# Kernel optimization log

Measured on AMD Instinct MI355X. Metric: run time of the kernel, lower is better.

Reference implementation:

```python
import jax, jax.numpy as jnp
import numpy as np

B, T, E = 512, 12, 1024   # batch, channels/seq, embed_dim
NH, HS = 8, 128           # num_heads, head_size (head_size=128 hard-coded in source)
H = NH * HS               # sLSTM hidden = 1024 (== E)


def _layer_norm(x, g, b, eps=1e-5):
    mu = x.mean(-1, keepdims=True)
    var = x.var(-1, keepdims=True)
    return (x - mu) * jax.lax.rsqrt(var + eps) * g + b


def _conv1d_same(x, w, b):
    # x: (B, C, L), w: (O, I, K) odd K, 'same' padding, stride 1
    k = w.shape[-1]
    p = (k - 1) // 2
    y = jax.lax.conv_general_dilated(x, w, (1,), [(p, p)],
                                     dimension_numbers=('NCH', 'OIH', 'NCH'))
    return y + b[None, :, None]


def setup_inputs():
    key = jax.random.key(0)
    ks = jax.random.split(key, 16)
    s = 0.02
    def nrm(k, shape, scale=s):
        return jax.random.normal(k, shape, jnp.float32) * scale
    return {
        'x': jax.random.normal(ks[0], (B, T, E), jnp.float32),
        'ln_g': jnp.ones((E,), jnp.float32), 'ln_b': jnp.zeros((E,), jnp.float32),
        'fc1_w': nrm(ks[1], (12, 12, 3)), 'fc1_b': jnp.zeros((12,), jnp.float32),
        'fc2_w': nrm(ks[2], (12, 12)), 'fc2_b': jnp.zeros((12,), jnp.float32),
        'conv1_w': nrm(ks[3], (48, 12, 3)), 'conv1_b': jnp.zeros((48,), jnp.float32),
        'conv2_w': nrm(ks[4], (12, 48, 3)), 'conv2_b': jnp.zeros((12,), jnp.float32),
        'xl_ln_g': jnp.ones((E,), jnp.float32), 'xl_ln_b': jnp.zeros((E,), jnp.float32),
        'Wg': nrm(ks[5], (E, 4 * H)), 'bg': jnp.zeros((4 * H,), jnp.float32),
        'Rg': nrm(ks[6], (NH, 4 * HS, HS)),
        'gn_g': jnp.ones((H,), jnp.float32), 'gn_b': jnp.zeros((H,), jnp.float32),
        'upl_w': nrm(ks[7], (H, H)), 'upl_b': jnp.zeros((H,), jnp.float32),
        'upr_w': nrm(ks[8], (H, H)), 'upr_b': jnp.zeros((H,), jnp.float32),
        'down_w': nrm(ks[9], (H, E)), 'down_b': jnp.zeros((E,), jnp.float32),
    }


def _slstm_block(x, xl_ln_g, xl_ln_b, Wg, bg, Rg, gn_g, gn_b,
                 upl_w, upl_b, upr_w, upr_b, down_w, down_b):
    # Stabilized multi-head sLSTM block: pre-LN -> sLSTM recurrence (exp i/f gates
    # with max-stabilizer m), per-head GroupNorm, gated up/down proj (proj_factor=1),
    # residual. Recurrent weights are block-diagonal per head (NH, 4*HS, HS).
    xn = _layer_norm(x, xl_ln_g, xl_ln_b)
    gx = jnp.einsum('bte,eg->btg', xn, Wg) + bg            # (B,T,4H) input gate pre-acts
    gx = jnp.swapaxes(gx, 0, 1)                            # (T,B,4H)

    def step(carry, g_t):
        h, c, n, m = carry                                 # each (B,NH,HS)
        rec = jnp.einsum('bnh,ngh->bng', h, Rg)            # (B,NH,4HS)
        g = g_t.reshape(g_t.shape[0], NH, 4 * HS) + rec
        z_, i_, f_, o_ = jnp.split(g, 4, axis=-1)
        z = jnp.tanh(z_)
        o = jax.nn.sigmoid(o_)
        m_new = jnp.maximum(f_ + m, i_)                    # log-space stabilizer
        i = jnp.exp(i_ - m_new)
        f = jnp.exp(f_ + m - m_new)
        c = f * c + i * z
        n = f * n + i
        h = o * (c / n)
        return (h, c, n, m_new), h

    zero = jnp.zeros((x.shape[0], NH, HS), x.dtype)
    _, hseq = jax.lax.scan(step, (zero, zero, zero, zero), gx)
    h = jnp.swapaxes(hseq, 0, 1)                           # (B,T,NH,HS)
    # GroupNorm(num_groups=NH) over each head's HS channels
    mu = h.mean(-1, keepdims=True)
    var = h.var(-1, keepdims=True)
    hn = (h - mu) * jax.lax.rsqrt(var + 1e-5)
    hn = hn.reshape(x.shape[0], x.shape[1], H) * gn_g + gn_b
    left = jax.nn.gelu(hn @ upl_w + upl_b, approximate=False)
    right = hn @ upr_w + upr_b
    return (left * right) @ down_w + down_b + x


def reference(x, ln_g, ln_b, fc1_w, fc1_b, fc2_w, fc2_b, conv1_w, conv1_b,
              conv2_w, conv2_b, xl_ln_g, xl_ln_b, Wg, bg, Rg, gn_g, gn_b,
              upl_w, upl_b, upr_w, upr_b, down_w, down_b):
    xn = _layer_norm(x, ln_g, ln_b)
    skip = xn
    xc = _conv1d_same(xn, fc1_w, fc1_b)                    # fc1: Conv1d(12,12,3,'same')
    x1 = jnp.einsum('bcl,oc->bol', xc, fc2_w) + fc2_b[None, :, None]  # fc2: 1x1 conv
    x1 = _slstm_block(x1, xl_ln_g, xl_ln_b, Wg, bg, Rg, gn_g, gn_b,
                      upl_w, upl_b, upr_w, upr_b, down_w, down_b)
    # dropout(0.2) is identity in eval mode
    y = jax.nn.silu(xc) * x1 + skip
    z = _conv1d_same(y, conv1_w, conv1_b)                  # 12 -> 48
    z = _layer_norm(jax.nn.gelu(z, approximate=False), ln_g, ln_b)
    z = _conv1d_same(z, conv2_w, conv2_b)                  # 48 -> 12
    return z + skip
```

## Files before the change

### kernel.cpp

```cpp
#include <hip/hip_runtime.h>
#include <math.h>


typedef short short8_t __attribute__((ext_vector_type(8)));
typedef float floatx4 __attribute__((ext_vector_type(4)));
typedef float float2_t __attribute__((ext_vector_type(2)));

typedef unsigned int u32;
typedef const __attribute__((address_space(1))) u32 gu32;
typedef __attribute__((address_space(3))) u32 lu32;

static __device__ __forceinline__ float b2f(unsigned short u) {
    unsigned v = ((unsigned)u) << 16;
    return __builtin_bit_cast(float, v);
}
static __device__ __forceinline__ unsigned short f2b(float f) {
    unsigned u = __builtin_bit_cast(unsigned, f);
    u += 0x7FFFu + ((u >> 16) & 1u);
    return (unsigned short)(u >> 16);
}
static __device__ __forceinline__ float2_t make2u(unsigned u) {
    float2_t r;
    r.x = __builtin_bit_cast(float, u << 16);
    r.y = __builtin_bit_cast(float, u & 0xFFFF0000u);
    return r;
}
static __device__ __forceinline__ u32 pack2(float a, float b) {
    return ((u32)f2b(b) << 16) | (u32)f2b(a);
}
static __device__ __forceinline__ float gelu_fast(float x) {
    float u = 0.7978845608f * x * (1.f + 0.044715f * x * x);
    u = fminf(fmaxf(u, -9.f), 9.f);
    return x * __builtin_amdgcn_rcpf(1.f + __expf(-2.f * u));
}


__global__ __launch_bounds__(256) void transpose_bf16_k(
    const float* __restrict__ src, unsigned short* __restrict__ dst,
    int K, int N, int GS, int GO)
{
    __shared__ unsigned short tl[32][33];
    const int n0 = blockIdx.x * 32, k0 = blockIdx.y * 32;
    const int tx = threadIdx.x & 31, ty = threadIdx.x >> 5;
#pragma unroll
    for (int r = 0; r < 4; r++) {
        int k = ty + r * 8;
        tl[tx][k] = f2b(src[(size_t)(k0 + k) * N + n0 + tx]);
    }
    __syncthreads();
#pragma unroll
    for (int r = 0; r < 4; r++) {
        int n = n0 + ty * 4 + r;
        size_t row = (size_t)((n >> 4) * GS + GO + (n & 15));
        dst[row * K + k0 + tx] = tl[ty * 4 + r][tx];
    }
}

__global__ __launch_bounds__(256) void bias_ilv_kernel(
    const float* __restrict__ bl, const float* __restrict__ br,
    float* __restrict__ o)
{
    int i = blockIdx.x * 256 + threadIdx.x;
    int grp = i >> 5, w = i & 31;
    o[i] = (w < 16) ? bl[grp * 16 + w] : br[grp * 16 + (w - 16)];
}


template <int BF16OUT>
__global__ __launch_bounds__(256) void ln_kernel(
    const float* __restrict__ in, const float* __restrict__ g,
    const float* __restrict__ be, void* __restrict__ outp)
{
    const int row = blockIdx.x;
    const float* xr = in + (size_t)row * 1024;
    const int t = threadIdx.x;
    float v[4];
    float s = 0.f, ss = 0.f;
#pragma unroll
    for (int u = 0; u < 4; u++) {
        float q = xr[t + u * 256];
        v[u] = q; s += q; ss += q * q;
    }
#pragma unroll
    for (int off = 32; off >= 1; off >>= 1) {
        s += __shfl_xor(s, off);
        ss += __shfl_xor(ss, off);
    }
    __shared__ float red[8];
    const int wv = t >> 6, la = t & 63;
    if (la == 0) { red[wv] = s; red[4 + wv] = ss; }
    __syncthreads();
    s = red[0] + red[1] + red[2] + red[3];
    ss = red[4] + red[5] + red[6] + red[7];
    float mu = s * (1.f / 1024.f);
    float var = ss * (1.f / 1024.f) - mu * mu;
    float rs = rsqrtf(var + 1e-5f);
#pragma unroll
    for (int u = 0; u < 4; u++) {
        int i = t + u * 256;
        float yv = (v[u] - mu) * rs * g[i] + be[i];
        if (BF16OUT)
            ((unsigned short*)outp)[(size_t)row * 1024 + i] = f2b(yv);
        else
            ((float*)outp)[(size_t)row * 1024 + i] = yv;
    }
}


__global__ __launch_bounds__(512, 3) void ln_fc_kernel(
    const float* __restrict__ x,
    const float* __restrict__ g, const float* __restrict__ be,
    const float* __restrict__ w1, const float* __restrict__ b1,
    const float* __restrict__ w2, const float* __restrict__ b2,
    float* __restrict__ xn, float* __restrict__ xc, float* __restrict__ x1)
{
    __shared__ float sX[12][1028];
    __shared__ float sMR[12][2];
    const int b = blockIdx.x;
    const int t = threadIdx.x;
    const int p = t;
    const size_t boff = (size_t)b * 12288;

    if (t < 12) { sX[t][0] = 0.f; sX[t][1025] = 0.f; sX[t][1026] = 0.f; sX[t][1027] = 0.f; }
    {
        const float* gx = x + boff;
#pragma unroll
        for (int ci = 0; ci < 12; ci++) {
            sX[ci][1 + p] = gx[ci * 1024 + p];
            sX[ci][1 + p + 512] = gx[ci * 1024 + p + 512];
        }
    }
    __syncthreads();

    {
        const int wv = t >> 6, la = t & 63;
#pragma unroll
        for (int j = 0; j < 2; j++) {
            const int ch = wv + j * 8;
            if (ch < 12) {
                float s = 0.f, ss = 0.f;
#pragma unroll
                for (int u = 0; u < 16; u++) {
                    float v = sX[ch][1 + la + u * 64];
                    s += v; ss += v * v;
                }
#pragma unroll
                for (int off = 32; off >= 1; off >>= 1) {
                    s += __shfl_xor(s, off);
                    ss += __shfl_xor(ss, off);
                }
                if (la == 0) {
                    float mu = s * (1.f / 1024.f);
                    float var = ss * (1.f / 1024.f) - mu * mu;
                    sMR[ch][0] = mu;
                    sMR[ch][1] = rsqrtf(var + 1e-5f);
                }
            }
        }
    }
    __syncthreads();

    const float gA = g[p], bA = be[p];
    const float gB = g[p + 512], bB = be[p + 512];
#pragma unroll
    for (int ch = 0; ch < 12; ch++) {
        const float mu = sMR[ch][0], rs = sMR[ch][1];
        float v0 = (sX[ch][1 + p] - mu) * rs * gA + bA;
        float v1 = (sX[ch][1 + p + 512] - mu) * rs * gB + bB;
        sX[ch][1 + p] = v0;
        sX[ch][1 + p + 512] = v1;
        xn[boff + (size_t)ch * 1024 + p] = v0;
        xn[boff + (size_t)ch * 1024 + p + 512] = v1;
    }
    __syncthreads();

    float2_t a1[12];
#pragma unroll
    for (int o = 0; o < 12; o++) { float bv = b1[o]; a1[o] = float2_t{bv, bv}; }
    for (int ci = 0; ci < 12; ci++) {
        float2_t vm = float2_t{sX[ci][p],     sX[ci][p + 512]};
        float2_t v0 = float2_t{sX[ci][p + 1], sX[ci][p + 513]};
        float2_t vp = float2_t{sX[ci][p + 2], sX[ci][p + 514]};
        const float* wp = w1 + ci * 3;
#pragma unroll
        for (int o = 0; o < 12; o++) {
            const float* wo = wp + o * 36;
            a1[o] += vm * wo[0] + v0 * wo[1] + vp * wo[2];
        }
    }
#pragma unroll
    for (int o = 0; o < 12; o++) {
        xc[boff + (size_t)o * 1024 + p] = a1[o].x;
        xc[boff + (size_t)o * 1024 + p + 512] = a1[o].y;
    }

    float2_t a2[12];
#pragma unroll
    for (int o = 0; o < 12; o++) { float bv = b2[o]; a2[o] = float2_t{bv, bv}; }
#pragma unroll
    for (int ci = 0; ci < 12; ci++) {
#pragma unroll
        for (int o = 0; o < 12; o++)
            a2[o] += a1[ci] * w2[o * 12 + ci];
    }
#pragma unroll
    for (int o = 0; o < 12; o++) {
        x1[boff + (size_t)o * 1024 + p] = a2[o].x;
        x1[boff + (size_t)o * 1024 + p + 512] = a2[o].y;
    }
}


template <int MODE>
__global__ __launch_bounds__(256) void gemm_kernel(
    const unsigned short* __restrict__ A, const unsigned short* __restrict__ BT,
    const float* __restrict__ bias, void* __restrict__ out,
    int M, int N, int K,
    const float* __restrict__ xc, const float* __restrict__ x1,
    const float* __restrict__ skip)
{
    __shared__ __align__(16) unsigned short sA[128 * 32];
    __shared__ __align__(16) unsigned short sB[128 * 32];
    const int t = threadIdx.x;
    const int m0 = blockIdx.y * 128;
    const int n0 = blockIdx.x * 128;
    const int w = t >> 6;
    const int lane = t & 63;
    const int wr = (w >> 1) * 64;
    const int wc = (w & 1) * 64;
    const int lrow = lane & 15;
    const int quad = lane >> 4;
    const int row_l = t >> 2;
    const int cs = (t & 3) * 8;

    const unsigned short* gA0 = A + (size_t)(m0 + row_l) * K + cs;
    const unsigned short* gA1 = A + (size_t)(m0 + row_l + 64) * K + cs;
    const unsigned short* gB0 = BT + (size_t)(n0 + row_l) * K + cs;
    const unsigned short* gB1 = BT + (size_t)(n0 + row_l + 64) * K + cs;
    unsigned short* lA0 = sA + w * 512;
    unsigned short* lA1 = sA + 2048 + w * 512;
    unsigned short* lB0 = sB + w * 512;
    unsigned short* lB1 = sB + 2048 + w * 512;

    floatx4 acc[4][4];
#pragma unroll
    for (int i = 0; i < 4; i++)
#pragma unroll
        for (int j = 0; j < 4; j++) acc[i][j] = (floatx4)0.f;

    for (int k0 = 0; k0 < K; k0 += 32) {
        __syncthreads();
        __builtin_amdgcn_global_load_lds((gu32*)(gA0 + k0), (lu32*)lA0, 16, 0, 0);
        __builtin_amdgcn_global_load_lds((gu32*)(gA1 + k0), (lu32*)lA1, 16, 0, 0);
        __builtin_amdgcn_global_load_lds((gu32*)(gB0 + k0), (lu32*)lB0, 16, 0, 0);
        __builtin_amdgcn_global_load_lds((gu32*)(gB1 + k0), (lu32*)lB1, 16, 0, 0);
        __syncthreads();
        short8_t af[4], bfr[4];
#pragma unroll
        for (int i = 0; i < 4; i++) {
            af[i] = *(const short8_t*)(sA + (wr + i * 16 + lrow) * 32 + quad * 8);
            bfr[i] = *(const short8_t*)(sB + (wc + i * 16 + lrow) * 32 + quad * 8);
        }
#pragma unroll
        for (int i = 0; i < 4; i++)
#pragma unroll
            for (int j = 0; j < 4; j++)
                acc[i][j] = __builtin_amdgcn_mfma_f32_16x16x32_bf16(
                    af[i], bfr[j], acc[i][j], 0, 0, 0);
    }

    if (MODE == 3) {
#pragma unroll
        for (int i = 0; i < 4; i++) {
#pragma unroll
            for (int k = 0; k < 2; k++) {
#pragma unroll
                for (int r = 0; r < 4; r++) {
                    const int gm = m0 + wr + i * 16 + quad * 4 + r;
                    const int pl = n0 + wc + k * 32 + lrow;
                    float lv = acc[i][2 * k][r] + bias[pl];
                    float rv = acc[i][2 * k + 1][r] + bias[pl + 16];
                    const int nlog = (pl >> 5) * 16 + lrow;
                    ((unsigned short*)out)[(size_t)gm * (N >> 1) + nlog] =
                        f2b(gelu_fast(lv) * rv);
                }
            }
        }
    } else {
#pragma unroll
        for (int i = 0; i < 4; i++) {
#pragma unroll
            for (int j = 0; j < 4; j++) {
#pragma unroll
                for (int r = 0; r < 4; r++) {
                    const int gm = m0 + wr + i * 16 + quad * 4 + r;
                    const int gn = n0 + wc + j * 16 + lrow;
                    const size_t idx = (size_t)gm * N + gn;
                    float v = acc[i][j][r] + bias[gn];
                    if (MODE == 0) {
                        ((unsigned short*)out)[idx] = f2b(v);
                    } else {
                        float xcv = xc[idx];
                        float sig = xcv * __builtin_amdgcn_rcpf(1.f + __expf(-xcv));
                        ((unsigned short*)out)[idx] =
                            f2b(sig * (v + x1[idx]) + skip[idx]);
                    }
                }
            }
        }
    }
}


#define RECP 516
#define HBP  136

__global__ __launch_bounds__(1024, 1) void slstm_rec_kernel(
    const float* __restrict__ Rg,
    const unsigned short* __restrict__ gxb,
    const float* __restrict__ gn_g, const float* __restrict__ gn_b,
    unsigned short* __restrict__ hnb)
{
    __shared__ __align__(16) float sRec[16 * RECP];
    __shared__ __align__(16) unsigned short sHb[16 * HBP];
    const int head = blockIdx.x;
    const int b0 = blockIdx.y * 16;
    const int t = threadIdx.x;
    const int w = t >> 6;
    const int lane = t & 63;
    const int quad = lane >> 4;
    const int l16 = lane & 15;

    short8_t Bf[2][4];
    {
        const float* Rh = Rg + (size_t)head * 65536;
#pragma unroll
        for (int jt = 0; jt < 2; jt++)
#pragma unroll
            for (int kk = 0; kk < 4; kk++) {
                const float* src =
                    Rh + (size_t)(w * 32 + jt * 16 + l16) * 128 + kk * 32 + quad * 8;
                short8_t v;
#pragma unroll
                for (int j = 0; j < 8; j++) v[j] = (short)f2b(src[j]);
                Bf[jt][kk] = v;
            }
    }

    for (int i = t; i < 16 * HBP; i += 1024) sHb[i] = 0;

    const int la = lane;
    float c0 = 0.f, n0s = 0.f, m0 = 0.f;
    float c1 = 0.f, n1s = 0.f, m1 = 0.f;
    const float gg0 = gn_g[head * 128 + la];
    const float gg1 = gn_g[head * 128 + la + 64];
    const float gb0 = gn_b[head * 128 + la];
    const float gb1 = gn_b[head * 128 + la + 64];

    __syncthreads();

    for (int step = 0; step < 12; step++) {
        const unsigned short* gp =
            gxb + ((size_t)(b0 + w) * 12 + step) * 4096 + head * 512;
        float gz0 = b2f(gp[la]),       gz1 = b2f(gp[64 + la]);
        float gi0 = b2f(gp[128 + la]), gi1 = b2f(gp[192 + la]);
        float gf0 = b2f(gp[256 + la]), gf1 = b2f(gp[320 + la]);
        float go0 = b2f(gp[384 + la]), go1 = b2f(gp[448 + la]);

        short8_t Af[4];
#pragma unroll
        for (int kk = 0; kk < 4; kk++)
            Af[kk] = *(const short8_t*)(sHb + l16 * HBP + kk * 32 + quad * 8);
        floatx4 D0 = (floatx4)0.f, D1 = (floatx4)0.f;
#pragma unroll
        for (int kk = 0; kk < 4; kk++) {
            D0 = __builtin_amdgcn_mfma_f32_16x16x32_bf16(Af[kk], Bf[0][kk], D0, 0, 0, 0);
            D1 = __builtin_amdgcn_mfma_f32_16x16x32_bf16(Af[kk], Bf[1][kk], D1, 0, 0, 0);
        }
#pragma unroll
        for (int r = 0; r < 4; r++) {
            sRec[(quad * 4 + r) * RECP + w * 32 + l16] = D0[r];
            sRec[(quad * 4 + r) * RECP + w * 32 + 16 + l16] = D1[r];
        }
        __syncthreads();

        const float* rr = sRec + w * RECP;
        float zp0 = gz0 + rr[la],       zp1 = gz1 + rr[64 + la];
        float ip0 = gi0 + rr[128 + la], ip1 = gi1 + rr[192 + la];
        float fp0 = gf0 + rr[256 + la], fp1 = gf1 + rr[320 + la];
        float op0 = go0 + rr[384 + la], op1 = go1 + rr[448 + la];

        float e20 = __expf(-2.f * zp0), e21 = __expf(-2.f * zp1);
        float z0 = 2.f * __builtin_amdgcn_rcpf(1.f + e20) - 1.f;
        float z1 = 2.f * __builtin_amdgcn_rcpf(1.f + e21) - 1.f;
        float o0 = __builtin_amdgcn_rcpf(1.f + __expf(-op0));
        float o1 = __builtin_amdgcn_rcpf(1.f + __expf(-op1));
        float mn0 = fmaxf(fp0 + m0, ip0), mn1 = fmaxf(fp1 + m1, ip1);
        float ie0 = __expf(ip0 - mn0), ie1 = __expf(ip1 - mn1);
        float fe0 = __expf(fp0 + m0 - mn0), fe1 = __expf(fp1 + m1 - mn1);
        c0 = fe0 * c0 + ie0 * z0;  c1 = fe1 * c1 + ie1 * z1;
        n0s = fe0 * n0s + ie0;     n1s = fe1 * n1s + ie1;
        m0 = mn0;                  m1 = mn1;
        float h0 = o0 * c0 * __builtin_amdgcn_rcpf(n0s);
        float h1 = o1 * c1 * __builtin_amdgcn_rcpf(n1s);

        float s = h0 + h1, ss = h0 * h0 + h1 * h1;
#pragma unroll
        for (int off = 32; off >= 1; off >>= 1) {
            s += __shfl_xor(s, off);
            ss += __shfl_xor(ss, off);
        }
        float mu = s * (1.f / 128.f);
        float var = ss * (1.f / 128.f) - mu * mu;
        float rs = rsqrtf(var + 1e-5f);
        size_t base = ((size_t)(b0 + w) * 12 + step) * 1024 + head * 128;
        hnb[base + la] = f2b((h0 - mu) * rs * gg0 + gb0);
        hnb[base + la + 64] = f2b((h1 - mu) * rs * gg1 + gb1);

        sHb[w * HBP + la] = f2b(h0);
        sHb[w * HBP + la + 64] = f2b(h1);
        __syncthreads();
    }
}


__global__ __launch_bounds__(512, 6) void tail_fused_kernel(
    const unsigned short* __restrict__ y, const float* __restrict__ skip,
    const float* __restrict__ w1, const float* __restrict__ b1,
    const float* __restrict__ w2, const float* __restrict__ b2,
    const float* __restrict__ lng, const float* __restrict__ lnb,
    float* __restrict__ out)
{
    __shared__ unsigned short sY[12][1026];
    __shared__ unsigned short sZ[12][1026];
    __shared__ float sMR[12][2];
    const int b = blockIdx.x;
    const int t = threadIdx.x;
    const int p = t;
    const size_t boff = (size_t)b * 12288;

    {
        const u32* gy = (const u32*)(y + boff);
#pragma unroll
        for (int ci = 0; ci < 12; ci++)
            ((u32*)&sY[ci][0])[t] = gy[ci * 512 + t];
    }
    const float lgA = lng[2 * t], lbA = lnb[2 * t];
    const float lgB = lng[2 * t + 1], lbB = lnb[2 * t + 1];
    __syncthreads();

    float2_t acc[12];
#pragma unroll
    for (int o = 0; o < 12; o++) { float bv = b2[o]; acc[o] = float2_t{bv, bv}; }

    for (int q = 0; q < 4; q++) {
        float2_t a1[12];
#pragma unroll
        for (int o = 0; o < 12; o++) {
            float bo = b1[q * 12 + o];
            a1[o] = float2_t{bo, bo};
        }
        for (int ci = 0; ci < 12; ci++) {
            float2_t v0 = float2_t{b2f(sY[ci][p]), b2f(sY[ci][p + 512])};
            float2_t vm = float2_t{(p > 0) ? b2f(sY[ci][p - 1]) : 0.f,
                                   b2f(sY[ci][p + 511])};
            float2_t vp = float2_t{b2f(sY[ci][p + 1]),
                                   (p < 511) ? b2f(sY[ci][p + 513]) : 0.f};
            const float* wp = w1 + ci * 3;
#pragma unroll
            for (int o = 0; o < 12; o++) {
                const float* wo = wp + (q * 12 + o) * 36;
                a1[o] += vm * wo[0] + v0 * wo[1] + vp * wo[2];
            }
        }
#pragma unroll
        for (int o = 0; o < 12; o++) {
            sZ[o][p] = f2b(gelu_fast(a1[o].x));
            sZ[o][p + 512] = f2b(gelu_fast(a1[o].y));
        }
        __syncthreads();

        {
            const int wv = t >> 6, la = t & 63;
#pragma unroll
            for (int j = 0; j < 2; j++) {
                const int ch = wv + j * 8;
                if (ch < 12) {
                    float s = 0.f, ss = 0.f;
#pragma unroll
                    for (int u = 0; u < 8; u++) {
                        float2_t v = make2u(((const u32*)&sZ[ch][0])[la + u * 64]);
                        s += v.x + v.y;
                        ss += v.x * v.x + v.y * v.y;
                    }
#pragma unroll
                    for (int off = 32; off >= 1; off >>= 1) {
                        s += __shfl_xor(s, off);
                        ss += __shfl_xor(ss, off);
                    }
                    if (la == 0) {
                        float mu = s * (1.f / 1024.f);
                        float var = ss * (1.f / 1024.f) - mu * mu;
                        sMR[ch][0] = mu;
                        sMR[ch][1] = rsqrtf(var + 1e-5f);
                    }
                }
            }
        }
        __syncthreads();

#pragma unroll
        for (int ch = 0; ch < 12; ch++) {
            const float mu = sMR[ch][0], rs = sMR[ch][1];
            float2_t f = make2u(((const u32*)&sZ[ch][0])[t]);
            f.x = (f.x - mu) * rs * lgA + lbA;
            f.y = (f.y - mu) * rs * lgB + lbB;
            ((u32*)&sZ[ch][0])[t] = pack2(f.x, f.y);
        }
        __syncthreads();

        for (int ci = 0; ci < 12; ci++) {
            float2_t z0 = float2_t{b2f(sZ[ci][p]), b2f(sZ[ci][p + 512])};
            float2_t zm = float2_t{(p > 0) ? b2f(sZ[ci][p - 1]) : 0.f,
                                   b2f(sZ[ci][p + 511])};
            float2_t zp = float2_t{b2f(sZ[ci][p + 1]),
                                   (p < 511) ? b2f(sZ[ci][p + 513]) : 0.f};
            const float* wp = w2 + (q * 12 + ci) * 3;
#pragma unroll
            for (int o = 0; o < 12; o++)
                acc[o] += zm * wp[o * 144] + z0 * wp[o * 144 + 1]
                        + zp * wp[o * 144 + 2];
        }
        __syncthreads();
    }

#pragma unroll
    for (int o = 0; o < 12; o++) {
        size_t i0 = boff + (size_t)o * 1024 + p;
        out[i0] = acc[o].x + skip[i0];
        out[i0 + 512] = acc[o].y + skip[i0 + 512];
    }
}


extern "C" void kernel_launch(void* const* d_in, const int* in_sizes, int n_in,
                              void* d_out, int out_size, void* d_ws, size_t ws_size,
                              hipStream_t stream)
{
    (void)in_sizes; (void)n_in; (void)out_size; (void)ws_size;
    const float* x      = (const float*)d_in[0];
    const float* ln_g   = (const float*)d_in[1];
    const float* ln_b   = (const float*)d_in[2];
    const float* fc1_w  = (const float*)d_in[3];
    const float* fc1_b  = (const float*)d_in[4];
    const float* fc2_w  = (const float*)d_in[5];
    const float* fc2_b  = (const float*)d_in[6];
    const float* conv1_w= (const float*)d_in[7];
    const float* conv1_b= (const float*)d_in[8];
    const float* conv2_w= (const float*)d_in[9];
    const float* conv2_b= (const float*)d_in[10];
    const float* xl_g   = (const float*)d_in[11];
    const float* xl_b   = (const float*)d_in[12];
    const float* Wg     = (const float*)d_in[13];
    const float* bg     = (const float*)d_in[14];
    const float* Rg     = (const float*)d_in[15];
    const float* gn_g   = (const float*)d_in[16];
    const float* gn_b   = (const float*)d_in[17];
    const float* upl_w  = (const float*)d_in[18];
    const float* upl_b  = (const float*)d_in[19];
    const float* upr_w  = (const float*)d_in[20];
    const float* upr_b  = (const float*)d_in[21];
    const float* down_w = (const float*)d_in[22];
    const float* down_b = (const float*)d_in[23];

    char* ws = (char*)d_ws;
    size_t off = 0;
    auto alloc = [&](size_t bytes) -> char* {
        char* p = ws + off;
        off = (off + bytes + 255) & ~(size_t)255;
        return p;
    };
    float* xn            = (float*)alloc(25165824);
    float* xc            = (float*)alloc(25165824);
    float* x1            = (float*)alloc(25165824);
    unsigned short* xn2b = (unsigned short*)alloc(12582912);
    unsigned short* gxb  = (unsigned short*)alloc(50331648);
    unsigned short* hnb  = (unsigned short*)alloc(12582912);
    unsigned short* glrb = (unsigned short*)alloc(12582912);
    unsigned short* yb   = (unsigned short*)alloc(12582912);
    unsigned short* WgT  = (unsigned short*)alloc(8388608);
    unsigned short* WupT = (unsigned short*)alloc(4194304);
    unsigned short* WdT  = (unsigned short*)alloc(2097152);
    float* bup           = (float*)alloc(8192);

    transpose_bf16_k<<<dim3(128, 32), 256, 0, stream>>>(Wg, WgT, 1024, 4096, 16, 0);
    transpose_bf16_k<<<dim3(32, 32), 256, 0, stream>>>(upl_w, WupT, 1024, 1024, 32, 0);
    transpose_bf16_k<<<dim3(32, 32), 256, 0, stream>>>(upr_w, WupT, 1024, 1024, 32, 16);
    transpose_bf16_k<<<dim3(32, 32), 256, 0, stream>>>(down_w, WdT, 1024, 1024, 16, 0);
    bias_ilv_kernel<<<8, 256, 0, stream>>>(upl_b, upr_b, bup);

    ln_fc_kernel<<<512, 512, 0, stream>>>(
        x, ln_g, ln_b, fc1_w, fc1_b, fc2_w, fc2_b, xn, xc, x1);
    ln_kernel<1><<<6144, 256, 0, stream>>>(x1, xl_g, xl_b, xn2b);
    gemm_kernel<0><<<dim3(32, 48), 256, 0, stream>>>(
        xn2b, WgT, bg, gxb, 6144, 4096, 1024, nullptr, nullptr, nullptr);
    slstm_rec_kernel<<<dim3(8, 32), 1024, 0, stream>>>(Rg, gxb, gn_g, gn_b, hnb);
    gemm_kernel<3><<<dim3(16, 48), 256, 0, stream>>>(
        hnb, WupT, bup, glrb, 6144, 2048, 1024, nullptr, nullptr, nullptr);
    gemm_kernel<2><<<dim3(8, 48), 256, 0, stream>>>(
        glrb, WdT, down_b, yb, 6144, 1024, 1024, xc, x1, xn);
    tail_fused_kernel<<<512, 512, 0, stream>>>(
        yb, xn, conv1_w, conv1_b, conv2_w, conv2_b, ln_g, ln_b, (float*)d_out);
}
```

Before: 450.2 us.

## Fuse sLSTM pre-LayerNorm into ln_fc kernel and double-buffer GEMM LDS loads

The separate LayerNorm kernel over x1 is folded into ln_fc_kernel. It reuses the shared tile to compute per-channel mean and rstd and writes the bf16 normalized output directly, which removes one launch and a full re-read of x1. Separately, the bf16 GEMM gets two LDS buffers so the next K-tile's global-to-LDS load is issued before the current tile's MFMAs, with one barrier per iteration. The trade-offs are extra LDS per GEMM block and a lower ln_fc occupancy bound (launch bounds 512,2).

```diff
diff --git a/kernel.cpp b/kernel.cpp
--- a/kernel.cpp
+++ b/kernel.cpp
@@ -66,53 +66,14 @@
 }
 
 
-template <int BF16OUT>
-__global__ __launch_bounds__(256) void ln_kernel(
-    const float* __restrict__ in, const float* __restrict__ g,
-    const float* __restrict__ be, void* __restrict__ outp)
-{
-    const int row = blockIdx.x;
-    const float* xr = in + (size_t)row * 1024;
-    const int t = threadIdx.x;
-    float v[4];
-    float s = 0.f, ss = 0.f;
-#pragma unroll
-    for (int u = 0; u < 4; u++) {
-        float q = xr[t + u * 256];
-        v[u] = q; s += q; ss += q * q;
-    }
-#pragma unroll
-    for (int off = 32; off >= 1; off >>= 1) {
-        s += __shfl_xor(s, off);
-        ss += __shfl_xor(ss, off);
-    }
-    __shared__ float red[8];
-    const int wv = t >> 6, la = t & 63;
-    if (la == 0) { red[wv] = s; red[4 + wv] = ss; }
-    __syncthreads();
-    s = red[0] + red[1] + red[2] + red[3];
-    ss = red[4] + red[5] + red[6] + red[7];
-    float mu = s * (1.f / 1024.f);
-    float var = ss * (1.f / 1024.f) - mu * mu;
-    float rs = rsqrtf(var + 1e-5f);
-#pragma unroll
-    for (int u = 0; u < 4; u++) {
-        int i = t + u * 256;
-        float yv = (v[u] - mu) * rs * g[i] + be[i];
-        if (BF16OUT)
-            ((unsigned short*)outp)[(size_t)row * 1024 + i] = f2b(yv);
-        else
-            ((float*)outp)[(size_t)row * 1024 + i] = yv;
-    }
-}
-
-
-__global__ __launch_bounds__(512, 3) void ln_fc_kernel(
+__global__ __launch_bounds__(512, 2) void ln_fc_kernel(
     const float* __restrict__ x,
     const float* __restrict__ g, const float* __restrict__ be,
+    const float* __restrict__ xlg, const float* __restrict__ xlb,
     const float* __restrict__ w1, const float* __restrict__ b1,
     const float* __restrict__ w2, const float* __restrict__ b2,
-    float* __restrict__ xn, float* __restrict__ xc, float* __restrict__ x1)
+    float* __restrict__ xn, float* __restrict__ xc, float* __restrict__ x1,
+    unsigned short* __restrict__ xn2b)
 {
     __shared__ float sX[12][1028];
     __shared__ float sMR[12][2];
@@ -188,6 +149,8 @@
             a1[o] += vm * wo[0] + v0 * wo[1] + vp * wo[2];
         }
     }
+    __syncthreads();
+
 #pragma unroll
     for (int o = 0; o < 12; o++) {
         xc[boff + (size_t)o * 1024 + p] = a1[o].x;
@@ -207,6 +170,48 @@
     for (int o = 0; o < 12; o++) {
         x1[boff + (size_t)o * 1024 + p] = a2[o].x;
         x1[boff + (size_t)o * 1024 + p + 512] = a2[o].y;
+        sX[o][p] = a2[o].x;
+        sX[o][p + 512] = a2[o].y;
+    }
+    __syncthreads();
+
+    {
+        const int wv = t >> 6, la = t & 63;
+#pragma unroll
+        for (int j = 0; j < 2; j++) {
+            const int ch = wv + j * 8;
+            if (ch < 12) {
+                float s = 0.f, ss = 0.f;
+#pragma unroll
+                for (int u = 0; u < 16; u++) {
+                    float v = sX[ch][la + u * 64];
+                    s += v; ss += v * v;
+                }
+#pragma unroll
+                for (int off = 32; off >= 1; off >>= 1) {
+                    s += __shfl_xor(s, off);
+                    ss += __shfl_xor(ss, off);
+                }
+                if (la == 0) {
+                    float mu = s * (1.f / 1024.f);
+                    float var = ss * (1.f / 1024.f) - mu * mu;
+                    sMR[ch][0] = mu;
+                    sMR[ch][1] = rsqrtf(var + 1e-5f);
+                }
+            }
+        }
+    }
+    __syncthreads();
+
+    const float xgA = xlg[p], xbA = xlb[p];
+    const float xgB = xlg[p + 512], xbB = xlb[p + 512];
+#pragma unroll
+    for (int ch = 0; ch < 12; ch++) {
+        const float mu = sMR[ch][0], rs = sMR[ch][1];
+        xn2b[boff + (size_t)ch * 1024 + p] =
+            f2b((a2[ch].x - mu) * rs * xgA + xbA);
+        xn2b[boff + (size_t)ch * 1024 + p + 512] =
+            f2b((a2[ch].y - mu) * rs * xgB + xbB);
     }
 }
 
@@ -219,8 +224,8 @@
     const float* __restrict__ xc, const float* __restrict__ x1,
     const float* __restrict__ skip)
 {
-    __shared__ __align__(16) unsigned short sA[128 * 32];
-    __shared__ __align__(16) unsigned short sB[128 * 32];
+    __shared__ __align__(16) unsigned short sA[2][128 * 32];
+    __shared__ __align__(16) unsigned short sB[2][128 * 32];
     const int t = threadIdx.x;
     const int m0 = blockIdx.y * 128;
     const int n0 = blockIdx.x * 128;
@@ -237,10 +242,6 @@
     const unsigned short* gA1 = A + (size_t)(m0 + row_l + 64) * K + cs;
     const unsigned short* gB0 = BT + (size_t)(n0 + row_l) * K + cs;
     const unsigned short* gB1 = BT + (size_t)(n0 + row_l + 64) * K + cs;
-    unsigned short* lA0 = sA + w * 512;
-    unsigned short* lA1 = sA + 2048 + w * 512;
-    unsigned short* lB0 = sB + w * 512;
-    unsigned short* lB1 = sB + 2048 + w * 512;
 
     floatx4 acc[4][4];
 #pragma unroll
@@ -248,26 +249,47 @@
 #pragma unroll
         for (int j = 0; j < 4; j++) acc[i][j] = (floatx4)0.f;
 
-    for (int k0 = 0; k0 < K; k0 += 32) {
+#define GEMM_STAGE(buf, k0)                                                        \
+    do {                                                                           \
+        __builtin_amdgcn_global_load_lds((gu32*)(gA0 + (k0)),                      \
+            (lu32*)(&sA[buf][w * 512]), 16, 0, 0);                                 \
+        __builtin_amdgcn_global_load_lds((gu32*)(gA1 + (k0)),                      \
+            (lu32*)(&sA[buf][2048 + w * 512]), 16, 0, 0);                          \
+        __builtin_amdgcn_global_load_lds((gu32*)(gB0 + (k0)),                      \
+            (lu32*)(&sB[buf][w * 512]), 16, 0, 0);                                 \
+        __builtin_amdgcn_global_load_lds((gu32*)(gB1 + (k0)),                      \
+            (lu32*)(&sB[buf][2048 + w * 512]), 16, 0, 0);                          \
+    } while (0)
+
+#define GEMM_COMPUTE(buf)                                                          \
+    do {                                                                           \
+        short8_t af[4], bfr[4];                                                    \
+        _Pragma("unroll")                                                          \
+        for (int i = 0; i < 4; i++) {                                              \
+            af[i] = *(const short8_t*)(&sA[buf][(wr + i * 16 + lrow) * 32 + quad * 8]); \
+            bfr[i] = *(const short8_t*)(&sB[buf][(wc + i * 16 + lrow) * 32 + quad * 8]); \
+        }                                                                          \
+        _Pragma("unroll")                                                          \
+        for (int i = 0; i < 4; i++)                                                \
+            _Pragma("unroll")                                                      \
+            for (int j = 0; j < 4; j++)                                            \
+                acc[i][j] = __builtin_amdgcn_mfma_f32_16x16x32_bf16(               \
+                    af[i], bfr[j], acc[i][j], 0, 0, 0);                            \
+    } while (0)
+
+    GEMM_STAGE(0, 0);
+    __syncthreads();
+    int cur = 0;
+    for (int k0 = 32; k0 < K; k0 += 32) {
+        GEMM_STAGE(cur ^ 1, k0);
+        GEMM_COMPUTE(cur);
         __syncthreads();
-        __builtin_amdgcn_global_load_lds((gu32*)(gA0 + k0), (lu32*)lA0, 16, 0, 0);
-        __builtin_amdgcn_global_load_lds((gu32*)(gA1 + k0), (lu32*)lA1, 16, 0, 0);
-        __builtin_amdgcn_global_load_lds((gu32*)(gB0 + k0), (lu32*)lB0, 16, 0, 0);
-        __builtin_amdgcn_global_load_lds((gu32*)(gB1 + k0), (lu32*)lB1, 16, 0, 0);
-        __syncthreads();
-        short8_t af[4], bfr[4];
-#pragma unroll
-        for (int i = 0; i < 4; i++) {
-            af[i] = *(const short8_t*)(sA + (wr + i * 16 + lrow) * 32 + quad * 8);
-            bfr[i] = *(const short8_t*)(sB + (wc + i * 16 + lrow) * 32 + quad * 8);
-        }
-#pragma unroll
-        for (int i = 0; i < 4; i++)
-#pragma unroll
-            for (int j = 0; j < 4; j++)
-                acc[i][j] = __builtin_amdgcn_mfma_f32_16x16x32_bf16(
-                    af[i], bfr[j], acc[i][j], 0, 0, 0);
-    }
+        cur ^= 1;
+    }
+    GEMM_COMPUTE(cur);
+
+#undef GEMM_STAGE
+#undef GEMM_COMPUTE
 
     if (MODE == 3) {
 #pragma unroll
@@ -600,8 +622,8 @@
     bias_ilv_kernel<<<8, 256, 0, stream>>>(upl_b, upr_b, bup);
 
     ln_fc_kernel<<<512, 512, 0, stream>>>(
-        x, ln_g, ln_b, fc1_w, fc1_b, fc2_w, fc2_b, xn, xc, x1);
-    ln_kernel<1><<<6144, 256, 0, stream>>>(x1, xl_g, xl_b, xn2b);
+        x, ln_g, ln_b, xl_g, xl_b, fc1_w, fc1_b, fc2_w, fc2_b,
+        xn, xc, x1, xn2b);
     gemm_kernel<0><<<dim3(32, 48), 256, 0, stream>>>(
         xn2b, WgT, bg, gxb, 6144, 4096, 1024, nullptr, nullptr, nullptr);
     slstm_rec_kernel<<<dim3(8, 32), 1024, 0, stream>>>(Rg, gxb, gn_g, gn_b, hnb);
```

Result: no change. 449.3 us (-0.2%).
